# Optimization experiments

Hardware: AMD Instinct MI355X
Metric: run time of the kernel (lower is better)

## Reference

```python
import jax, jax.numpy as jnp
import numpy as np

B, N, F, FOBS, D = 4, 1024, 128, 32, 128
K_HOP = 3  # os.environ k_hop default 3


def setup_inputs() -> dict:
    key = jax.random.key(0)
    k0, k1, k2, k3, k4 = jax.random.split(key, 5)
    X = jax.random.normal(k0, (B, N, F), jnp.float32)
    # xavier-ish scales for params
    a_link = jax.random.normal(k1, (FOBS, 1), jnp.float32) * (1.414 / np.sqrt(FOBS + 1))
    W0 = jax.random.normal(k2, (F, D), jnp.float32) * np.sqrt(2.0 / (F + D))
    W1 = jax.random.normal(k3, (D, D), jnp.float32) * np.sqrt(1.0 / D)
    W2 = jax.random.normal(k4, (D, D), jnp.float32) * np.sqrt(1.0 / D)
    return {"X": X, "a_link": a_link, "W0": W0, "W1": W1, "W2": W2}


def reference(X, a_link, W0, W1, W2):
    eye = jnp.eye(N, dtype=X.dtype)

    def per_graph(Xb):  # Xb: [N, F]
        h = Xb[:, :FOBS]                                   # [N, FOBS]
        # e_ij = a_link^T |h_i - h_j|
        e = jnp.einsum('ijf,fo->ij', jnp.abs(h[:, None, :] - h[None, :, :]), a_link)
        A = jax.nn.sigmoid(e)
        A = A * (1.0 - eye)                                # zero diagonal (A - diag(diag(A)))
        Dm = jnp.zeros_like(A)                             # diag(diag(A)) is zero after removal
        A_hat = A + eye
        d_inv_sqrt = jnp.sum(A_hat, axis=1) ** -0.5        # row sums (dim=1 in mini_batch path)
        norm = d_inv_sqrt[:, None] * A_hat * d_inv_sqrt[None, :]  # D^-1/2 A_hat D^-1/2
        H = norm @ (Xb @ W0)                               # k = 0
        for Wk in (W1, W2):                                # k = 1 .. K_HOP-1 (norm detached in torch)
            H = jax.lax.stop_gradient(norm) @ (H @ Wk)
        return jax.nn.relu(H), A, Dm

    Hs, As, Ds = jax.vmap(per_graph)(X)
    return Hs, As, X, Ds
```

## Files before the change

kernel.cpp:

```cpp
#include <hip/hip_runtime.h>
#include <math.h>

#define BB 4
#define NN 1024
#define FF 128
#define DD 128
#define FOBS 32

typedef __attribute__((ext_vector_type(8))) short bfrag;
typedef __attribute__((ext_vector_type(4))) float ffrag;
typedef __attribute__((ext_vector_type(4))) unsigned short us4;

__device__ __forceinline__ unsigned short f2bf(float x) {
    unsigned u = __builtin_bit_cast(unsigned, x);
    u += 0x7fffu + ((u >> 16) & 1u);
    return (unsigned short)(u >> 16);
}
__device__ __forceinline__ void gload16(const void* g, void* l) {
    __builtin_amdgcn_global_load_lds((const __attribute__((address_space(1))) unsigned*)g,
                                     (__attribute__((address_space(3))) unsigned*)l, 16, 0, 0);
}

__global__ __launch_bounds__(256) void zero_f4(float4* __restrict__ p, int n4) {
    int i = blockIdx.x * 256 + threadIdx.x;
    if (i < n4) p[i] = make_float4(0.f, 0.f, 0.f, 0.f);
}

__global__ __launch_bounds__(256) void adj_kernel(const float* __restrict__ X,
                                                  const float* __restrict__ a_link,
                                                  const float* __restrict__ W0,
                                                  const float* __restrict__ W1,
                                                  const float* __restrict__ W2,
                                                  float* __restrict__ As,
                                                  unsigned short* __restrict__ Xbf,
                                                  unsigned short* __restrict__ W01t,
                                                  unsigned short* __restrict__ W2t,
                                                  float* __restrict__ Pp,
                                                  float* __restrict__ Xo,
                                                  float* __restrict__ Zd) {
    int tid = threadIdx.x;
    if (blockIdx.z == 5) {
        if (Zd) {
            int q = blockIdx.y * 16 + blockIdx.x;
            float4* Z = (float4*)Zd;
#pragma unroll
            for (int p = 0; p < 16; p++)
                Z[(size_t)q * 4096 + p * 256 + tid] = make_float4(0.f, 0.f, 0.f, 0.f);
        }
        return;
    }
    if (blockIdx.z == 4) {
        int q = (blockIdx.y * 16 + blockIdx.x) * 256 + tid;
        if (q < 16384) {
            int g = q >> 7, f = q & 127;
            float s = 0.f;
            for (int h = 0; h < 128; h++) s += W0[f * 128 + h] * W1[h * 128 + g];
            W01t[q] = f2bf(s);
        } else if (q < 32768) {
            int e = q - 16384;
            int f2 = e >> 7, g = e & 127;
            W2t[e] = f2bf(W2[g * 128 + f2]);
        } else {
            int u = q - 32768;
#pragma unroll
            for (int p = 0; p < 4; p++) {
                size_t i4 = (size_t)u + (size_t)p * 32768;
                float4 v = *(const float4*)&X[i4 * 4];
                us4 o; o[0] = f2bf(v.x); o[1] = f2bf(v.y); o[2] = f2bf(v.z); o[3] = f2bf(v.w);
                *(us4*)&Xbf[i4 * 4] = o;
            }
        }
        return;
    }
    int b = blockIdx.z, i0 = blockIdx.y * 64, j0 = blockIdx.x * 64;
    __shared__ float hi[64][FOBS + 1];
    __shared__ float hj[64][FOBS + 1];
    __shared__ float av[FOBS];
    __shared__ float part_s[64][16];
    const float* Xb = X + (size_t)b * NN * FF;
    if (j0 == 0) {
#pragma unroll
        for (int p = 0; p < 8; p++) {
            int c = p * 256 + tid, r = c >> 5, qq = c & 31;
            *(float4*)&Xo[((size_t)b * NN + i0 + r) * FF + qq * 4] =
                *(const float4*)&Xb[(size_t)(i0 + r) * FF + qq * 4];
        }
    }
#pragma unroll
    for (int l = 0; l < 8; l++) {
        int idx = l * 256 + tid;
        int r = idx >> 5, f = idx & 31;
        hi[r][f] = Xb[(size_t)(i0 + r) * FF + f];
        hj[r][f] = Xb[(size_t)(j0 + r) * FF + f];
    }
    if (tid < FOBS) av[tid] = a_link[tid];
    __syncthreads();

    int ty = tid >> 4, tx = tid & 15;
    int ir = ty * 4, jc = tx * 4;
    float acc[4][4] = {};
#pragma unroll
    for (int f = 0; f < FOBS; f++) {
        float a = av[f];
        float x[4], y[4];
#pragma unroll
        for (int r = 0; r < 4; r++) x[r] = hi[ir + r][f];
#pragma unroll
        for (int c = 0; c < 4; c++) y[c] = hj[jc + c][f];
#pragma unroll
        for (int r = 0; r < 4; r++)
#pragma unroll
            for (int c = 0; c < 4; c++)
                acc[r][c] += fabsf(x[r] - y[c]) * a;
    }
    float* Ab = As + (size_t)b * NN * NN;
#pragma unroll
    for (int r = 0; r < 4; r++) {
        int gi = i0 + ir + r;
        float vv[4]; float rs = 0.f;
#pragma unroll
        for (int c = 0; c < 4; c++) {
            int gj = j0 + jc + c;
            float sg = 1.f / (1.f + __expf(-acc[r][c]));
            vv[c] = (gi == gj) ? 0.f : sg;
            rs += vv[c];
        }
        *(float4*)&Ab[(size_t)gi * NN + (j0 + jc)] = make_float4(vv[0], vv[1], vv[2], vv[3]);
        part_s[ir + r][tx] = rs;
    }
    __syncthreads();
    if (tid < 64) {
        float s = 0.f;
#pragma unroll
        for (int k = 0; k < 16; k++) s += part_s[tid][k];
        Pp[((size_t)b * NN + i0 + tid) * 16 + blockIdx.x] = s;
    }
}

__global__ __launch_bounds__(256) void t0_kernel(const unsigned short* __restrict__ Xbf,
                                                 const unsigned short* __restrict__ W01t,
                                                 const unsigned short* __restrict__ W2t,
                                                 const float* __restrict__ Pp,
                                                 unsigned short* __restrict__ TtX,
                                                 float* __restrict__ dinvG) {
    int bid = blockIdx.x;
    int b = bid >> 6, n0 = (bid & 63) * 16;
    __shared__ unsigned short W01s[128 * 128];
    __shared__ unsigned short W2s[128 * 128];
    __shared__ unsigned short Xps[16 * 128];
    __shared__ unsigned short Ps[16 * 128];
    int tid = threadIdx.x;
    const unsigned short* Xb = Xbf + (size_t)b * NN * DD;
#pragma unroll
    for (int p = 0; p < 8; p++) {
        int c = p * 256 + tid, row = c >> 4, kc = c & 15;
        gload16(W01t + (size_t)row * 128 + ((kc ^ (row & 7)) * 8), W01s + (size_t)c * 8);
    }
#pragma unroll
    for (int p = 0; p < 8; p++) {
        int c = p * 256 + tid, row = c >> 4, kc = c & 15;
        gload16(W2t + (size_t)row * 128 + ((kc ^ (row & 7)) * 8), W2s + (size_t)c * 8);
    }
    {
        int c = tid, row = c >> 4, kc = c & 15;
        gload16(Xb + (size_t)(n0 + row) * 128 + ((kc ^ (row & 7)) * 8), Xps + (size_t)c * 8);
    }
    {
        int r = tid >> 4, p = tid & 15;
        float s = Pp[((size_t)b * NN + n0 + r) * 16 + p];
        s += __shfl_xor(s, 1);
        s += __shfl_xor(s, 2);
        s += __shfl_xor(s, 4);
        s += __shfl_xor(s, 8);
        if (p == 0) dinvG[(size_t)b * NN + n0 + r] = rsqrtf(1.f + s);
    }
    __syncthreads();

    int w = tid >> 6, l = tid & 63, lr = l & 15, lg = l >> 4;
    ffrag pacc[2] = {};
#pragma unroll
    for (int ks = 0; ks < 4; ks++) {
        int k0 = ks * 32 + lg * 8;
        bfrag a[2], bb;
#pragma unroll
        for (int rb = 0; rb < 2; rb++) {
            int row = w * 32 + rb * 16 + lr;
            int byt = (row * 256 + k0 * 2) ^ ((row & 7) << 4);
            a[rb] = *(const bfrag*)((const char*)W01s + byt);
        }
        {
            int byt = (lr * 256 + k0 * 2) ^ ((lr & 7) << 4);
            bb = *(const bfrag*)((const char*)Xps + byt);
        }
#pragma unroll
        for (int rb = 0; rb < 2; rb++)
            pacc[rb] = __builtin_amdgcn_mfma_f32_16x16x32_bf16(a[rb], bb, pacc[rb], 0, 0, 0);
    }
#pragma unroll
    for (int rb = 0; rb < 2; rb++) {
        int g0 = w * 32 + rb * 16 + lg * 4;
        us4 o;
#pragma unroll
        for (int r = 0; r < 4; r++) o[r] = f2bf(pacc[rb][r]);
        int byt = (lr * 256 + g0 * 2) ^ ((lr & 7) << 4);
        *(us4*)((char*)Ps + byt) = o;
    }
    __syncthreads();
    ffrag tacc[2] = {};
#pragma unroll
    for (int ks = 0; ks < 4; ks++) {
        int k0 = ks * 32 + lg * 8;
        bfrag a2[2], b2;
#pragma unroll
        for (int rb = 0; rb < 2; rb++) {
            int row = w * 32 + rb * 16 + lr;
            int byt = (row * 256 + k0 * 2) ^ ((row & 7) << 4);
            a2[rb] = *(const bfrag*)((const char*)W2s + byt);
        }
        {
            int byt = (lr * 256 + k0 * 2) ^ ((lr & 7) << 4);
            b2 = *(const bfrag*)((const char*)Ps + byt);
        }
#pragma unroll
        for (int rb = 0; rb < 2; rb++)
            tacc[rb] = __builtin_amdgcn_mfma_f32_16x16x32_bf16(a2[rb], b2, tacc[rb], 0, 0, 0);
    }
    unsigned short* Tb = TtX + (size_t)b * DD * NN;
#pragma unroll
    for (int rb = 0; rb < 2; rb++)
#pragma unroll
        for (int r = 0; r < 4; r++) {
            int f2 = w * 32 + rb * 16 + lg * 4 + r;
            Tb[(size_t)f2 * NN + n0 + lr] = f2bf(tacc[rb][r]);
        }
}

template <int LAST>
__global__ __launch_bounds__(256) void ga_kernel(const float* __restrict__ As,
                                                 const float* __restrict__ dinvG,
                                                 const unsigned short* __restrict__ Tin,
                                                 unsigned short* __restrict__ Tout,
                                                 float* __restrict__ HsF) {
    int bid = blockIdx.x;
    int b = bid >> 6, n0 = (bid & 63) * 16;
    __shared__ unsigned short T_s[3 * 128 * 64];
    __shared__ unsigned short S_s[16 * 1024];
    __shared__ float dinvF[NN];
    int tid = threadIdx.x;
    const unsigned short* Tb = Tin + (size_t)b * DD * NN;

    auto stageT = [&](int buf, int kt) {
#pragma unroll
        for (int p = 0; p < 4; p++) {
            int c = p * 256 + tid, row = c >> 3, kc = c & 7;
            gload16(Tb + (size_t)row * NN + kt + ((kc ^ (row & 7)) * 8),
                    T_s + (size_t)buf * (128 * 64) + (size_t)c * 8);
        }
    };
    stageT(0, 0);
    stageT(1, 64);

    {
        *(float4*)&dinvF[tid * 4] = *(const float4*)&dinvG[(size_t)b * NN + tid * 4];
    }
    __syncthreads();
    {
        int row = tid >> 4, gi = n0 + row;
        const float* Ar = As + ((size_t)b * NN + gi) * NN;
        float di = dinvF[gi];
#pragma unroll
        for (int cc = 0; cc < 16; cc++) {
            int col = (tid & 15) * 4 + cc * 64;
            float4 a4 = *(const float4*)&Ar[col];
            us4 o;
            o[0] = f2bf(di * dinvF[col + 0] * (a4.x + ((col + 0) == gi ? 1.f : 0.f)));
            o[1] = f2bf(di * dinvF[col + 1] * (a4.y + ((col + 1) == gi ? 1.f : 0.f)));
            o[2] = f2bf(di * dinvF[col + 2] * (a4.z + ((col + 2) == gi ? 1.f : 0.f)));
            o[3] = f2bf(di * dinvF[col + 3] * (a4.w + ((col + 3) == gi ? 1.f : 0.f)));
            int byt = (row * 2048 + col * 2) ^ ((row & 7) << 4);
            *(us4*)((char*)S_s + byt) = o;
        }
    }
    __syncthreads();

    int w = tid >> 6, l = tid & 63, lr = l & 15, lg = l >> 4;
    ffrag acc[2] = {};
    int cur = 0, sb = 2;
    for (int t = 0; t < 16; t++) {
        if (t <= 13) stageT(sb, (t + 2) * 64);
        if (t < 14)       asm volatile("s_waitcnt vmcnt(8)" ::: "memory");
        else if (t == 14) asm volatile("s_waitcnt vmcnt(4)" ::: "memory");
        else              asm volatile("s_waitcnt vmcnt(0)" ::: "memory");
        __builtin_amdgcn_s_barrier();
        asm volatile("" ::: "memory");
        const unsigned short* Tc = T_s + (size_t)cur * (128 * 64);
#pragma unroll
        for (int ks = 0; ks < 2; ks++) {
            int k0 = ks * 32 + lg * 8;
            int kg = t * 64 + k0;
            bfrag a[2], bb;
#pragma unroll
            for (int rb = 0; rb < 2; rb++) {
                int row = w * 32 + rb * 16 + lr;
                int byt = (row * 128 + k0 * 2) ^ ((row & 7) << 4);
                a[rb] = *(const bfrag*)((const char*)Tc + byt);
            }
            {
                int byt = (lr * 2048 + kg * 2) ^ ((lr & 7) << 4);
                bb = *(const bfrag*)((const char*)S_s + byt);
            }
#pragma unroll
            for (int rb = 0; rb < 2; rb++)
                acc[rb] = __builtin_amdgcn_mfma_f32_16x16x32_bf16(a[rb], bb, acc[rb], 0, 0, 0);
        }
        asm volatile("s_waitcnt lgkmcnt(0)" ::: "memory");
        __builtin_amdgcn_s_barrier();
        cur = (cur == 2) ? 0 : cur + 1;
        sb = (sb == 2) ? 0 : sb + 1;
    }

    if (LAST) {
#pragma unroll
        for (int rb = 0; rb < 2; rb++) {
            int f0 = w * 32 + rb * 16 + lg * 4;
            float v[4];
#pragma unroll
            for (int r = 0; r < 4; r++) v[r] = fmaxf(acc[rb][r], 0.f);
            *(float4*)&HsF[((size_t)b * NN + n0 + lr) * DD + f0] = make_float4(v[0], v[1], v[2], v[3]);
        }
    } else {
        unsigned short* Ob = Tout + (size_t)b * DD * NN;
#pragma unroll
        for (int rb = 0; rb < 2; rb++)
#pragma unroll
            for (int r = 0; r < 4; r++) {
                int f = w * 32 + rb * 16 + lg * 4 + r;
                Ob[(size_t)f * NN + n0 + lr] = f2bf(acc[rb][r]);
            }
    }
}

extern "C" void kernel_launch(void* const* d_in, const int* in_sizes, int n_in,
                              void* d_out, int out_size, void* d_ws, size_t ws_size,
                              hipStream_t stream) {
    const float* X      = (const float*)d_in[0];
    const float* a_link = (const float*)d_in[1];
    const float* W0     = (const float*)d_in[2];
    const float* W1     = (const float*)d_in[3];
    const float* W2     = (const float*)d_in[4];
    float* out = (float*)d_out;

    const size_t HND = (size_t)BB * NN * DD;
    const size_t HNN = (size_t)BB * NN * NN;
    float* Hs = out;
    float* As = out + HND;
    float* Xo = out + HND + HNN;
    float* Ds = out + 2 * HND + HNN;

    const size_t NEED = 3489792;
    bool usews = (ws_size >= NEED);
    char* scr = usews ? (char*)d_ws : (char*)Ds;

    unsigned short* Xbf  = (unsigned short*)(scr);
    unsigned short* TtX  = (unsigned short*)(scr + 1048576);
    unsigned short* TtY  = (unsigned short*)(scr + 2097152);
    unsigned short* W01t = (unsigned short*)(scr + 3145728);
    unsigned short* W2t  = (unsigned short*)(scr + 3178496);
    float* Pp            = (float*)(scr + 3211264);
    float* dinvG         = (float*)(scr + 3473408);

    adj_kernel<<<dim3(16, 16, usews ? 6 : 5), 256, 0, stream>>>(
        X, a_link, W0, W1, W2, As, Xbf, W01t, W2t, Pp, Xo, usews ? Ds : nullptr);
    t0_kernel<<<dim3(256), 256, 0, stream>>>(Xbf, W01t, W2t, Pp, TtX, dinvG);
    ga_kernel<0><<<dim3(256), 256, 0, stream>>>(As, dinvG, TtX, TtY, nullptr);
    ga_kernel<0><<<dim3(256), 256, 0, stream>>>(As, dinvG, TtY, TtX, nullptr);
    ga_kernel<1><<<dim3(256), 256, 0, stream>>>(As, dinvG, TtX, nullptr, Hs);

    if (!usews)
        zero_f4<<<dim3(4096), 256, 0, stream>>>((float4*)Ds, (int)(HNN / 4));
}
```

Baseline: 56.66 us.

## Stream bf16 adjacency and fold symmetric normalization into T scaling

```diff
diff --git a/kernel.cpp b/kernel.cpp
--- a/kernel.cpp
+++ b/kernel.cpp
@@ -15,6 +15,10 @@
     unsigned u = __builtin_bit_cast(unsigned, x);
     u += 0x7fffu + ((u >> 16) & 1u);
     return (unsigned short)(u >> 16);
+}
+__device__ __forceinline__ float bf2f(unsigned short s) {
+    unsigned u = (unsigned)s << 16;
+    return __builtin_bit_cast(float, u);
 }
 __device__ __forceinline__ void gload16(const void* g, void* l) {
     __builtin_amdgcn_global_load_lds((const __attribute__((address_space(1))) unsigned*)g,
@@ -32,6 +36,7 @@
                                                   const float* __restrict__ W1,
                                                   const float* __restrict__ W2,
                                                   float* __restrict__ As,
+                                                  unsigned short* __restrict__ Abf,
                                                   unsigned short* __restrict__ Xbf,
                                                   unsigned short* __restrict__ W01t,
                                                   unsigned short* __restrict__ W2t,
@@ -114,6 +119,7 @@
                 acc[r][c] += fabsf(x[r] - y[c]) * a;
     }
     float* Ab = As + (size_t)b * NN * NN;
+    unsigned short* Abb = Abf + (size_t)b * NN * NN;
 #pragma unroll
     for (int r = 0; r < 4; r++) {
         int gi = i0 + ir + r;
@@ -126,6 +132,8 @@
             rs += vv[c];
         }
         *(float4*)&Ab[(size_t)gi * NN + (j0 + jc)] = make_float4(vv[0], vv[1], vv[2], vv[3]);
+        us4 o; o[0] = f2bf(vv[0]); o[1] = f2bf(vv[1]); o[2] = f2bf(vv[2]); o[3] = f2bf(vv[3]);
+        *(us4*)&Abb[(size_t)gi * NN + (j0 + jc)] = o;
         part_s[ir + r][tx] = rs;
     }
     __syncthreads();
@@ -141,30 +149,16 @@
                                                  const unsigned short* __restrict__ W01t,
                                                  const unsigned short* __restrict__ W2t,
                                                  const float* __restrict__ Pp,
-                                                 unsigned short* __restrict__ TtX,
-                                                 float* __restrict__ dinvG) {
+                                                 unsigned short* __restrict__ TtX) {
     int bid = blockIdx.x;
     int b = bid >> 6, n0 = (bid & 63) * 16;
     __shared__ unsigned short W01s[128 * 128];
     __shared__ unsigned short W2s[128 * 128];
     __shared__ unsigned short Xps[16 * 128];
     __shared__ unsigned short Ps[16 * 128];
+    __shared__ float dinv_s[16];
     int tid = threadIdx.x;
     const unsigned short* Xb = Xbf + (size_t)b * NN * DD;
-#pragma unroll
-    for (int p = 0; p < 8; p++) {
-        int c = p * 256 + tid, row = c >> 4, kc = c & 15;
-        gload16(W01t + (size_t)row * 128 + ((kc ^ (row & 7)) * 8), W01s + (size_t)c * 8);
-    }
-#pragma unroll
-    for (int p = 0; p < 8; p++) {
-        int c = p * 256 + tid, row = c >> 4, kc = c & 15;
-        gload16(W2t + (size_t)row * 128 + ((kc ^ (row & 7)) * 8), W2s + (size_t)c * 8);
-    }
-    {
-        int c = tid, row = c >> 4, kc = c & 15;
-        gload16(Xb + (size_t)(n0 + row) * 128 + ((kc ^ (row & 7)) * 8), Xps + (size_t)c * 8);
-    }
     {
         int r = tid >> 4, p = tid & 15;
         float s = Pp[((size_t)b * NN + n0 + r) * 16 + p];
@@ -172,7 +166,21 @@
         s += __shfl_xor(s, 2);
         s += __shfl_xor(s, 4);
         s += __shfl_xor(s, 8);
-        if (p == 0) dinvG[(size_t)b * NN + n0 + r] = rsqrtf(1.f + s);
+        if (p == 0) dinv_s[r] = rsqrtf(1.f + s);
+    }
+#pragma unroll
+    for (int p = 0; p < 8; p++) {
+        int c = p * 256 + tid, row = c >> 4, kc = c & 15;
+        gload16(W01t + (size_t)row * 128 + ((kc ^ (row & 7)) * 8), W01s + (size_t)c * 8);
+    }
+#pragma unroll
+    for (int p = 0; p < 8; p++) {
+        int c = p * 256 + tid, row = c >> 4, kc = c & 15;
+        gload16(W2t + (size_t)row * 128 + ((kc ^ (row & 7)) * 8), W2s + (size_t)c * 8);
+    }
+    {
+        int c = tid, row = c >> 4, kc = c & 15;
+        gload16(Xb + (size_t)(n0 + row) * 128 + ((kc ^ (row & 7)) * 8), Xps + (size_t)c * 8);
     }
     __syncthreads();
 
@@ -226,92 +234,82 @@
             tacc[rb] = __builtin_amdgcn_mfma_f32_16x16x32_bf16(a2[rb], b2, tacc[rb], 0, 0, 0);
     }
     unsigned short* Tb = TtX + (size_t)b * DD * NN;
+    float dv = dinv_s[lr];
 #pragma unroll
     for (int rb = 0; rb < 2; rb++)
 #pragma unroll
         for (int r = 0; r < 4; r++) {
             int f2 = w * 32 + rb * 16 + lg * 4 + r;
-            Tb[(size_t)f2 * NN + n0 + lr] = f2bf(tacc[rb][r]);
+            Tb[(size_t)f2 * NN + n0 + lr] = f2bf(tacc[rb][r] * dv);
         }
 }
 
 template <int LAST>
-__global__ __launch_bounds__(256) void ga_kernel(const float* __restrict__ As,
-                                                 const float* __restrict__ dinvG,
+__global__ __launch_bounds__(256) void ga_kernel(const unsigned short* __restrict__ Abf,
+                                                 const float* __restrict__ Pp,
                                                  const unsigned short* __restrict__ Tin,
                                                  unsigned short* __restrict__ Tout,
                                                  float* __restrict__ HsF) {
     int bid = blockIdx.x;
-    int b = bid >> 6, n0 = (bid & 63) * 16;
-    __shared__ unsigned short T_s[3 * 128 * 64];
-    __shared__ unsigned short S_s[16 * 1024];
-    __shared__ float dinvF[NN];
+    int fh = bid & 1, panel = bid >> 1;
+    int b = panel >> 6, n0 = (panel & 63) * 16;
+    __shared__ unsigned short T_s[3 * 64 * 64];
+    __shared__ unsigned short A_s[3 * 16 * 64];
+    __shared__ float dinv_s[16];
     int tid = threadIdx.x;
-    const unsigned short* Tb = Tin + (size_t)b * DD * NN;
-
+    const unsigned short* TbF = Tin + (size_t)b * DD * NN;
+    const unsigned short* Tb  = TbF + (size_t)fh * 64 * NN;
+    const unsigned short* Ab  = Abf + (size_t)b * NN * NN;
+
+    {
+        int r = tid >> 4, p = tid & 15;
+        float s = Pp[((size_t)b * NN + n0 + r) * 16 + p];
+        s += __shfl_xor(s, 1);
+        s += __shfl_xor(s, 2);
+        s += __shfl_xor(s, 4);
+        s += __shfl_xor(s, 8);
+        if (p == 0) dinv_s[r] = rsqrtf(1.f + s);
+    }
     auto stageT = [&](int buf, int kt) {
 #pragma unroll
-        for (int p = 0; p < 4; p++) {
+        for (int p = 0; p < 2; p++) {
             int c = p * 256 + tid, row = c >> 3, kc = c & 7;
             gload16(Tb + (size_t)row * NN + kt + ((kc ^ (row & 7)) * 8),
-                    T_s + (size_t)buf * (128 * 64) + (size_t)c * 8);
-        }
+                    T_s + (size_t)buf * (64 * 64) + (size_t)c * 8);
+        }
+        int c = tid & 127, row = c >> 3, kc = c & 7;
+        gload16(Ab + (size_t)(n0 + row) * NN + kt + ((kc ^ (row & 7)) * 8),
+                A_s + (size_t)buf * (16 * 64) + (size_t)c * 8);
     };
     stageT(0, 0);
     stageT(1, 64);
 
-    {
-        *(float4*)&dinvF[tid * 4] = *(const float4*)&dinvG[(size_t)b * NN + tid * 4];
-    }
-    __syncthreads();
-    {
-        int row = tid >> 4, gi = n0 + row;
-        const float* Ar = As + ((size_t)b * NN + gi) * NN;
-        float di = dinvF[gi];
-#pragma unroll
-        for (int cc = 0; cc < 16; cc++) {
-            int col = (tid & 15) * 4 + cc * 64;
-            float4 a4 = *(const float4*)&Ar[col];
-            us4 o;
-            o[0] = f2bf(di * dinvF[col + 0] * (a4.x + ((col + 0) == gi ? 1.f : 0.f)));
-            o[1] = f2bf(di * dinvF[col + 1] * (a4.y + ((col + 1) == gi ? 1.f : 0.f)));
-            o[2] = f2bf(di * dinvF[col + 2] * (a4.z + ((col + 2) == gi ? 1.f : 0.f)));
-            o[3] = f2bf(di * dinvF[col + 3] * (a4.w + ((col + 3) == gi ? 1.f : 0.f)));
-            int byt = (row * 2048 + col * 2) ^ ((row & 7) << 4);
-            *(us4*)((char*)S_s + byt) = o;
-        }
-    }
-    __syncthreads();
-
     int w = tid >> 6, l = tid & 63, lr = l & 15, lg = l >> 4;
-    ffrag acc[2] = {};
+    ffrag acc = {};
     int cur = 0, sb = 2;
     for (int t = 0; t < 16; t++) {
         if (t <= 13) stageT(sb, (t + 2) * 64);
-        if (t < 14)       asm volatile("s_waitcnt vmcnt(8)" ::: "memory");
-        else if (t == 14) asm volatile("s_waitcnt vmcnt(4)" ::: "memory");
+        if (t < 14)       asm volatile("s_waitcnt vmcnt(6)" ::: "memory");
+        else if (t == 14) asm volatile("s_waitcnt vmcnt(3)" ::: "memory");
         else              asm volatile("s_waitcnt vmcnt(0)" ::: "memory");
         __builtin_amdgcn_s_barrier();
         asm volatile("" ::: "memory");
-        const unsigned short* Tc = T_s + (size_t)cur * (128 * 64);
+        const unsigned short* Tc = T_s + (size_t)cur * (64 * 64);
+        const unsigned short* Ac = A_s + (size_t)cur * (16 * 64);
 #pragma unroll
         for (int ks = 0; ks < 2; ks++) {
             int k0 = ks * 32 + lg * 8;
-            int kg = t * 64 + k0;
-            bfrag a[2], bb;
-#pragma unroll
-            for (int rb = 0; rb < 2; rb++) {
-                int row = w * 32 + rb * 16 + lr;
+            bfrag a, bb;
+            {
+                int row = w * 16 + lr;
                 int byt = (row * 128 + k0 * 2) ^ ((row & 7) << 4);
-                a[rb] = *(const bfrag*)((const char*)Tc + byt);
+                a = *(const bfrag*)((const char*)Tc + byt);
             }
             {
-                int byt = (lr * 2048 + kg * 2) ^ ((lr & 7) << 4);
-                bb = *(const bfrag*)((const char*)S_s + byt);
+                int byt = (lr * 128 + k0 * 2) ^ ((lr & 7) << 4);
+                bb = *(const bfrag*)((const char*)Ac + byt);
             }
-#pragma unroll
-            for (int rb = 0; rb < 2; rb++)
-                acc[rb] = __builtin_amdgcn_mfma_f32_16x16x32_bf16(a[rb], bb, acc[rb], 0, 0, 0);
+            acc = __builtin_amdgcn_mfma_f32_16x16x32_bf16(a, bb, acc, 0, 0, 0);
         }
         asm volatile("s_waitcnt lgkmcnt(0)" ::: "memory");
         __builtin_amdgcn_s_barrier();
@@ -319,24 +317,25 @@
         sb = (sb == 2) ? 0 : sb + 1;
     }
 
+    int nl = lr;
+    float dv = dinv_s[nl];
+    int f0 = fh * 64 + w * 16 + lg * 4;
     if (LAST) {
-#pragma unroll
-        for (int rb = 0; rb < 2; rb++) {
-            int f0 = w * 32 + rb * 16 + lg * 4;
-            float v[4];
-#pragma unroll
-            for (int r = 0; r < 4; r++) v[r] = fmaxf(acc[rb][r], 0.f);
-            *(float4*)&HsF[((size_t)b * NN + n0 + lr) * DD + f0] = make_float4(v[0], v[1], v[2], v[3]);
-        }
+        float v[4];
+#pragma unroll
+        for (int r = 0; r < 4; r++) {
+            float idv = bf2f(TbF[(size_t)(f0 + r) * NN + n0 + nl]);
+            v[r] = fmaxf((acc[r] + idv) * dv, 0.f);
+        }
+        *(float4*)&HsF[((size_t)b * NN + n0 + nl) * DD + f0] = make_float4(v[0], v[1], v[2], v[3]);
     } else {
+        float dv2 = dv * dv;
         unsigned short* Ob = Tout + (size_t)b * DD * NN;
 #pragma unroll
-        for (int rb = 0; rb < 2; rb++)
-#pragma unroll
-            for (int r = 0; r < 4; r++) {
-                int f = w * 32 + rb * 16 + lg * 4 + r;
-                Ob[(size_t)f * NN + n0 + lr] = f2bf(acc[rb][r]);
-            }
+        for (int r = 0; r < 4; r++) {
+            float idv = bf2f(TbF[(size_t)(f0 + r) * NN + n0 + nl]);
+            Ob[(size_t)(f0 + r) * NN + n0 + nl] = f2bf((acc[r] + idv) * dv2);
+        }
     }
 }
 
@@ -357,24 +356,24 @@
     float* Xo = out + HND + HNN;
     float* Ds = out + 2 * HND + HNN;
 
-    const size_t NEED = 3489792;
+    const size_t NEED = 11862016;
     bool usews = (ws_size >= NEED);
     char* scr = usews ? (char*)d_ws : (char*)Ds;
 
-    unsigned short* Xbf  = (unsigned short*)(scr);
-    unsigned short* TtX  = (unsigned short*)(scr + 1048576);
-    unsigned short* TtY  = (unsigned short*)(scr + 2097152);
-    unsigned short* W01t = (unsigned short*)(scr + 3145728);
-    unsigned short* W2t  = (unsigned short*)(scr + 3178496);
-    float* Pp            = (float*)(scr + 3211264);
-    float* dinvG         = (float*)(scr + 3473408);
+    unsigned short* Abf  = (unsigned short*)(scr);
+    unsigned short* Xbf  = (unsigned short*)(scr + 8388608);
+    unsigned short* TtX  = (unsigned short*)(scr + 9437184);
+    unsigned short* TtY  = (unsigned short*)(scr + 10485760);
+    unsigned short* W01t = (unsigned short*)(scr + 11534336);
+    unsigned short* W2t  = (unsigned short*)(scr + 11567104);
+    float* Pp            = (float*)(scr + 11599872);
 
     adj_kernel<<<dim3(16, 16, usews ? 6 : 5), 256, 0, stream>>>(
-        X, a_link, W0, W1, W2, As, Xbf, W01t, W2t, Pp, Xo, usews ? Ds : nullptr);
-    t0_kernel<<<dim3(256), 256, 0, stream>>>(Xbf, W01t, W2t, Pp, TtX, dinvG);
-    ga_kernel<0><<<dim3(256), 256, 0, stream>>>(As, dinvG, TtX, TtY, nullptr);
-    ga_kernel<0><<<dim3(256), 256, 0, stream>>>(As, dinvG, TtY, TtX, nullptr);
-    ga_kernel<1><<<dim3(256), 256, 0, stream>>>(As, dinvG, TtX, nullptr, Hs);
+        X, a_link, W0, W1, W2, As, Abf, Xbf, W01t, W2t, Pp, Xo, usews ? Ds : nullptr);
+    t0_kernel<<<dim3(256), 256, 0, stream>>>(Xbf, W01t, W2t, Pp, TtX);
+    ga_kernel<0><<<dim3(512), 256, 0, stream>>>(Abf, Pp, TtX, TtY, nullptr);
+    ga_kernel<0><<<dim3(512), 256, 0, stream>>>(Abf, Pp, TtY, TtX, nullptr);
+    ga_kernel<1><<<dim3(512), 256, 0, stream>>>(Abf, Pp, TtX, nullptr, Hs);
 
     if (!usews)
         zero_f4<<<dim3(4096), 256, 0, stream>>>((float4*)Ds, (int)(HNN / 4));
```

Result: faster. 50.54 us (-10.8%).
